# Kernel optimization log

Hardware: AMD Instinct MI355X
Metric: run time of the kernel (lower is better)

## Reference

```python
import jax, jax.numpy as jnp
import numpy as np

KS = 3   # kernel_size
PAD = 1  # padding
N_K = KS * KS


def conv2d(x, w, b=None, stride=1, pad=0):
    out = jax.lax.conv_general_dilated(
        x, w, (stride, stride), [(pad, pad), (pad, pad)],
        dimension_numbers=('NCHW', 'OIHW', 'NCHW'))
    if b is not None:
        out = out + b[None, :, None, None]
    return out


def deform_sample(x, offset):
    # x: [b,c,H,W]  offset: [b,2N,h,w] -> [b,c,h,w,N]
    b, c, H, W = x.shape
    _, twoN, h, w = offset.shape
    N = twoN // 2
    xp = jnp.pad(x, ((0, 0), (0, 0), (PAD, PAD), (PAD, PAD)))
    Hp, Wp = H + 2 * PAD, W + 2 * PAD
    r = (KS - 1) // 2
    knx, kny = jnp.meshgrid(jnp.arange(-r, r + 1), jnp.arange(-r, r + 1), indexing='ij')
    pnx = knx.reshape(-1).astype(offset.dtype)  # [N] kernel x offsets
    pny = kny.reshape(-1).astype(offset.dtype)
    off = jnp.transpose(offset, (0, 2, 3, 1))   # [b,h,w,2N]
    p0x = (jnp.arange(h) + PAD).astype(offset.dtype)
    p0y = (jnp.arange(w) + PAD).astype(offset.dtype)
    px = p0x[None, :, None, None] + pnx[None, None, None, :] + off[..., :N]  # [b,h,w,N]
    py = p0y[None, None, :, None] + pny[None, None, None, :] + off[..., N:]
    # q = p.detach().floor() in torch -> stop_gradient here
    flx = jnp.floor(jax.lax.stop_gradient(px))
    fly = jnp.floor(jax.lax.stop_gradient(py))
    qltx = jnp.clip(flx, 0, Hp - 1)
    qrbx = jnp.clip(flx + 1, 0, Hp - 1)
    qlty = jnp.clip(fly, 0, Wp - 1)
    qrby = jnp.clip(fly + 1, 0, Wp - 1)
    pxc = jnp.clip(px, 0, Hp - 1)
    pyc = jnp.clip(py, 0, Wp - 1)
    g_lt = (1 + (qltx - pxc)) * (1 + (qlty - pyc))
    g_rb = (1 - (qrbx - pxc)) * (1 - (qrby - pyc))
    g_lb = (1 - (qrbx - pxc)) * (1 + (qlty - pyc))
    g_rt = (1 + (qltx - pxc)) * (1 - (qrby - pyc))
    ix_lt, ix_rb = qltx.astype(jnp.int32), qrbx.astype(jnp.int32)
    iy_lt, iy_rb = qlty.astype(jnp.int32), qrby.astype(jnp.int32)

    def gather(ix, iy):
        def one(xb, ixb, iyb):
            return xb[:, ixb, iyb]  # [c,h,w,N]
        return jax.vmap(one)(xp, ix, iy)

    x_lt = gather(ix_lt, iy_lt)
    x_rb = gather(ix_rb, iy_rb)
    x_lb = gather(ix_rb, iy_lt)
    x_rt = gather(ix_lt, iy_rb)
    return (g_lt[:, None] * x_lt + g_rb[:, None] * x_rb
            + g_lb[:, None] * x_lb + g_rt[:, None] * x_rt)


def z_weight(z, mode):
    # cubic interpolation basis weights; z: [b,N,h,w] -> [b,1,h,w,N]
    if mode == '1':
        w = 1 - 11.0 / 6.0 * z + z ** 2 - 1.0 / 6.0 * z ** 3
    elif mode == '2':
        w = 3 * z - 2.5 * z ** 2 + 0.5 * z ** 3
    elif mode == '4':
        w = -1.5 * z + 2 * z ** 2 - 0.5 * z ** 3
    else:
        w = 1.0 / 3.0 * z - 0.5 * z ** 2 + 1.0 / 6.0 * z ** 3
    return jnp.transpose(w, (0, 2, 3, 1))[:, None]


def reshape_x_offset(xo):
    # [b,c,h,w,ks*ks] -> [b,c,h*ks,w*ks] (torch cat/view equivalent)
    b, c, h, w, _ = xo.shape
    xo = xo.reshape(b, c, h, w, KS, KS)          # N = g*ks + k
    xo = jnp.transpose(xo, (0, 1, 2, 4, 3, 5))   # (b,c,h,g,w,k)
    return xo.reshape(b, c, h * KS, w * KS)


def setup_inputs() -> dict:
    key = jax.random.key(0)
    ks = jax.random.split(key, 18)
    B, C, OSC, OUTC, H, W = 2, 64, 64, 64, 128, 128
    f = jax.random.normal
    inp = {
        'img1': f(ks[0], (B, C, H, W), jnp.float32),
        'img2': f(ks[1], (B, C, H, W), jnp.float32),
        'img4': f(ks[2], (B, C, H, W), jnp.float32),
        'img5': f(ks[3], (B, C, H, W), jnp.float32),
        'offset_source': f(ks[4], (B, OSC, H, W), jnp.float32),
        'w_pc1': f(ks[5], (2 * N_K, OSC, 5, 5), jnp.float32) * 0.01,
        'b_pc1': f(ks[6], (2 * N_K,), jnp.float32) * 0.01,
        'w_pc2': f(ks[7], (2 * N_K, OSC, 5, 5), jnp.float32) * 0.01,
        'b_pc2': f(ks[8], (2 * N_K,), jnp.float32) * 0.01,
        'w_pc4': f(ks[9], (2 * N_K, OSC, 5, 5), jnp.float32) * 0.01,
        'b_pc4': f(ks[10], (2 * N_K,), jnp.float32) * 0.01,
        'w_pc5': f(ks[11], (2 * N_K, OSC, 5, 5), jnp.float32) * 0.01,
        'b_pc5': f(ks[12], (2 * N_K,), jnp.float32) * 0.01,
        'w_z': f(ks[13], (N_K, OSC, 5, 5), jnp.float32) * 0.01,
        'b_z': f(ks[14], (N_K,), jnp.float32) * 0.01,
        'w_m': f(ks[15], (N_K, OSC, 5, 5), jnp.float32) * 0.01,
        'b_m': f(ks[16], (N_K,), jnp.float32) * 0.01,
        'w_conv': f(ks[17], (OUTC, C, KS, KS), jnp.float32) * 0.05,
    }
    return inp


def reference(img1, img2, img4, img5, offset_source,
              w_pc1, b_pc1, w_pc2, b_pc2, w_pc4, b_pc4, w_pc5, b_pc5,
              w_z, b_z, w_m, b_m, w_conv):
    off1 = conv2d(offset_source, w_pc1, b_pc1, pad=2)
    off2 = conv2d(offset_source, w_pc2, b_pc2, pad=2)
    off4 = conv2d(offset_source, w_pc4, b_pc4, pad=2)
    off5 = conv2d(offset_source, w_pc5, b_pc5, pad=2)
    z = 3.0 * jax.nn.sigmoid(conv2d(offset_source, w_z, b_z, pad=2))
    m = jax.nn.sigmoid(conv2d(offset_source, w_m, b_m, pad=2))
    f1 = deform_sample(img1, off1)
    f2 = deform_sample(img2, off2)
    f4 = deform_sample(img4, off4)
    f5 = deform_sample(img5, off5)
    central = (f1 * z_weight(z, '1') + f2 * z_weight(z, '2')
               + f4 * z_weight(z, '4') + f5 * z_weight(z, '5'))
    central = central * jnp.transpose(m, (0, 2, 3, 1))[:, None]
    out = conv2d(reshape_x_offset(central), w_conv, None, stride=KS)
    return out
```

## Files before the change

kernel.cpp:

```cpp
#include <hip/hip_runtime.h>
#include <hip/hip_bf16.h>
#include <math.h>

#define HWX 16384

typedef __attribute__((ext_vector_type(8))) short short8v;
typedef __attribute__((ext_vector_type(4))) float f32x4;

__device__ inline ushort f2bf(float x) {
    union { __hip_bfloat16 h; ushort u; } cv;
    cv.h = __float2bfloat16(x);
    return cv.u;
}

__global__ __launch_bounds__(256) void prep_kernel(
    const float* __restrict__ w1, const float* __restrict__ b1,
    const float* __restrict__ w2, const float* __restrict__ b2,
    const float* __restrict__ w4, const float* __restrict__ b4,
    const float* __restrict__ w5, const float* __restrict__ b5,
    const float* __restrict__ wz, const float* __restrict__ bz,
    const float* __restrict__ wm, const float* __restrict__ bm,
    const float* __restrict__ osrc, const float* __restrict__ wc,
    __hip_bfloat16* __restrict__ Wpk, float* __restrict__ bpack,
    __hip_bfloat16* __restrict__ osT, __hip_bfloat16* __restrict__ WcPk)
{
    const int bid = blockIdx.x;
    if (bid < 600) {
        const int idx = bid * 256 + threadIdx.x;
        if (idx < 96) {
            const int o = idx; float v = 0.f;
            if      (o < 18) v = b1[o];
            else if (o < 36) v = b2[o - 18];
            else if (o < 54) v = b4[o - 36];
            else if (o < 72) v = b5[o - 54];
            else if (o < 81) v = bz[o - 72];
            else if (o < 90) v = bm[o - 81];
            bpack[o] = v;
        }
        if (idx < 96 * 1600) {
            const int o   = idx / 1600;
            const int k   = idx - o * 1600;
            const int kyx = k >> 6;
            const int ic  = k & 63;
            const int off = ic * 25 + kyx;
            float v = 0.f;
            if      (o < 18) v = w1[o * 1600 + off];
            else if (o < 36) v = w2[(o - 18) * 1600 + off];
            else if (o < 54) v = w4[(o - 36) * 1600 + off];
            else if (o < 72) v = w5[(o - 54) * 1600 + off];
            else if (o < 81) v = wz[(o - 72) * 1600 + off];
            else if (o < 90) v = wm[(o - 81) * 1600 + off];
            Wpk[idx] = __float2bfloat16(v);
        }
    } else if (bid < 864) {
        const int blk = bid - 600;
        const int yy = blk % 132;
        const int b  = blk / 132;
        __hip_bfloat16* dst = osT + ((size_t)b * 132 + yy) * 132 * 64;
        for (int idx = threadIdx.x; idx < 132 * 64; idx += 256) {
            const int xx = idx >> 6;
            const int c  = idx & 63;
            float v = 0.f;
            if (yy >= 2 && yy < 130 && xx >= 2 && xx < 130)
                v = osrc[(((b << 6) + c) << 14) + ((yy - 2) << 7) + (xx - 2)];
            dst[idx] = __float2bfloat16(v);
        }
    } else {
        const int idx = (bid - 864) * 256 + threadIdx.x;
        if (idx < 36864) {
            const int oc  = idx / 576;
            const int cnp = idx - oc * 576;
            const int n   = cnp >> 6;
            const int c   = cnp & 63;
            WcPk[idx] = __float2bfloat16(wc[oc * 576 + c * 9 + n]);
        }
    }
}

__global__ __launch_bounds__(256) void conv_mfma_kernel(
    const __hip_bfloat16* __restrict__ Wpk,
    const float* __restrict__ bpack,
    const __hip_bfloat16* __restrict__ osT,
    float* __restrict__ offs, float* __restrict__ zbuf, float* __restrict__ mbuf)
{
    __shared__ __align__(16) ushort slab[5 * 68 * 64];
    __shared__ __align__(16) ushort wbuf[2][96 * 64];

    const int bx = blockIdx.x;
    const int y  = bx >> 1;
    const int x0 = (bx & 1) << 6;
    const int b  = blockIdx.y;
    const int t    = threadIdx.x;
    const int wv   = t >> 6;
    const int lane = t & 63;
    const int l15  = lane & 15;
    const int kgrp = lane >> 4;
    const int wm   = wv >> 1;
    const int wn   = wv & 1;

    const ushort* ob = (const ushort*)osT + (size_t)b * (132 * 132 * 64);
    const ushort* Wg = (const ushort*)Wpk;

    for (int c = t; c < 2720; c += 256) {
        const int r5  = c / 544;
        const int rem = c - r5 * 544;
        const int col = rem >> 3;
        const int cb  = rem & 7;
        const short8v v = *(const short8v*)(ob + (((y + r5) * 132 + x0 + col) << 6) + (cb << 3));
        const int slot = r5 * 544 + (col << 3) + (cb ^ (col & 7));
        *(short8v*)((char*)slab + slot * 16) = v;
    }

#define STAGE_W(kyx, bi)                                                       \
    _Pragma("unroll")                                                          \
    for (int it = 0; it < 3; ++it) {                                           \
        const int c  = it * 256 + t;                                           \
        const int oc = c >> 3, cb = c & 7;                                     \
        const ushort* src = Wg + oc * 1600 + (kyx) * 64 + ((cb ^ (oc & 7)) << 3); \
        __builtin_amdgcn_global_load_lds(                                      \
            (const __attribute__((address_space(1))) void*)src,                \
            (__attribute__((address_space(3))) void*)((char*)wbuf[bi] + (it * 256 + wv * 64) * 16), \
            16, 0, 0);                                                         \
    }

    STAGE_W(0, 0)
    __syncthreads();

    f32x4 acc[3][2];
    #pragma unroll
    for (int m = 0; m < 3; ++m)
        #pragma unroll
        for (int n = 0; n < 2; ++n) acc[m][n] = (f32x4){0.f, 0.f, 0.f, 0.f};

    for (int kyx = 0; kyx < 25; ++kyx) {
        const int bi = kyx & 1;
        if (kyx < 24) STAGE_W(kyx + 1, bi ^ 1)
        const int ky = kyx / 5, kx = kyx % 5;
        #pragma unroll
        for (int kc = 0; kc < 2; ++kc) {
            const int kcg = (kc << 2) + kgrp;
            short8v af[3], bf[2];
            #pragma unroll
            for (int m = 0; m < 3; ++m) {
                const int oc = wm * 48 + m * 16 + l15;
                af[m] = *(const short8v*)((char*)wbuf[bi] + ((oc << 3) + (kcg ^ (oc & 7))) * 16);
            }
            #pragma unroll
            for (int n = 0; n < 2; ++n) {
                const int col = wn * 32 + n * 16 + l15 + kx;
                bf[n] = *(const short8v*)((char*)slab + ((ky * 68 + col) * 8 + (kcg ^ (col & 7))) * 16);
            }
            #pragma unroll
            for (int m = 0; m < 3; ++m)
                #pragma unroll
                for (int n = 0; n < 2; ++n)
                    acc[m][n] = __builtin_amdgcn_mfma_f32_16x16x32_bf16(af[m], bf[n], acc[m][n], 0, 0, 0);
        }
        __syncthreads();
    }
#undef STAGE_W

    #pragma unroll
    for (int m = 0; m < 3; ++m) {
        const int ocb = wm * 48 + m * 16 + (kgrp << 2);
        #pragma unroll
        for (int n = 0; n < 2; ++n) {
            const int x = x0 + wn * 32 + n * 16 + l15;
            const int p = (y << 7) + x;
            #pragma unroll
            for (int r = 0; r < 4; ++r) {
                const int o = ocb + r;
                const float v = acc[m][n][r] + bpack[o];
                if (o < 72) {
                    const int i = o / 18, ch = o - i * 18;
                    offs[i * (2 * 18 * HWX) + (((b * 18) + ch) << 14) + p] = v;
                } else if (o < 81) {
                    zbuf[((b * 9 + (o - 72)) << 14) + p] = 3.f / (1.f + expf(-v));
                } else if (o < 90) {
                    mbuf[((b * 9 + (o - 81)) << 14) + p] = 1.f / (1.f + expf(-v));
                }
            }
        }
    }
}

__global__ __launch_bounds__(256) void transpose_kernel(
    const float* __restrict__ i0, const float* __restrict__ i1,
    const float* __restrict__ i2, const float* __restrict__ i3,
    ushort* __restrict__ imgT)
{
    const int img = blockIdx.z;
    const int b   = blockIdx.y;
    const int p0  = blockIdx.x << 6;
    const float* src = (img == 0) ? i0 : (img == 1) ? i1 : (img == 2) ? i2 : i3;

    __shared__ float tile[64][65];
    const int t = threadIdx.x;
    const int pp = t & 63, c0 = t >> 6;
    #pragma unroll
    for (int k = 0; k < 16; ++k) {
        const int c = (k << 2) + c0;
        tile[c][pp] = src[(((b << 6) + c) << 14) + p0 + pp];
    }
    __syncthreads();
    const int c2 = t & 31, pl = t >> 5;
    #pragma unroll
    for (int k = 0; k < 8; ++k) {
        const int pi = (k << 3) + pl;
        const uint packed = (uint)f2bf(tile[2 * c2][pi])
                          | ((uint)f2bf(tile[2 * c2 + 1][pi]) << 16);
        *(uint*)(imgT + ((size_t)(((img << 1) + b) << 14) + p0 + pi) * 64 + 2 * c2)
            = packed;
    }
}

__global__ __launch_bounds__(256, 5) void fused_kernel(
    const float* __restrict__ offs,
    const float* __restrict__ zbuf,
    const float* __restrict__ mbuf,
    const ushort* __restrict__ imgT,
    const __hip_bfloat16* __restrict__ WcPk,
    float* __restrict__ out)
{
    __shared__ __hip_bfloat16 s_sb[16 * 584];
    __shared__ uint4 s_tap[16 * 36];

    const int t   = threadIdx.x;
    const int pid = blockIdx.x;
    const int b   = pid >> 10;
    const int rem = pid & 1023;
    const int h   = rem >> 3;
    const int w0p = (rem & 7) << 4;

    for (int u = t; u < 576; u += 256) {
        const int px_  = u / 36;
        const int unit = u - px_ * 36;
        const int i    = unit / 9;
        const int n    = unit - i * 9;
        const int wcol = w0p + px_;
        const int p    = (h << 7) + wcol;

        const float* ob = offs + i * (2 * 18 * HWX) + ((b * 18) << 14);
        const float ox = ob[(n << 14) + p];
        const float oy = ob[((n + 9) << 14) + p];
        const float z  = zbuf[((b * 9 + n) << 14) + p];
        const float mm = mbuf[((b * 9 + n) << 14) + p];

        const float zc0 = (i == 0) ? 1.f : 0.f;
        const float zc1 = (i == 0) ? (-11.f / 6.f) : (i == 1) ? 3.f
                         : (i == 2) ? -1.5f : (1.f / 3.f);
        const float zc2 = (i == 0) ? 1.f : (i == 1) ? -2.5f
                         : (i == 2) ? 2.f : -0.5f;
        const float zc3 = (i == 0) ? (-1.f / 6.f) : (i == 1) ? 0.5f
                         : (i == 2) ? -0.5f : (1.f / 6.f);
        const float zw   = zc0 + z * (zc1 + z * (zc2 + z * zc3));
        const float coef = zw * mm;

        const float pxf = (float)(h + n / 3) + ox;
        const float pyf = (float)(wcol + n % 3) + oy;
        const float flx = floorf(pxf), fly = floorf(pyf);
        const float qltx = fminf(fmaxf(flx, 0.f), 129.f);
        const float qrbx = fminf(fmaxf(flx + 1.f, 0.f), 129.f);
        const float qlty = fminf(fmaxf(fly, 0.f), 129.f);
        const float qrby = fminf(fmaxf(fly + 1.f, 0.f), 129.f);
        const float pxc = fminf(fmaxf(pxf, 0.f), 129.f);
        const float pyc = fminf(fmaxf(pyf, 0.f), 129.f);
        const float gxl = 1.f + (qltx - pxc);
        const float gxr = 1.f - (qrbx - pxc);
        const float gyl = 1.f + (qlty - pyc);
        const float gyr = 1.f - (qrby - pyc);
        const int ixl = (int)qltx, ixr = (int)qrbx;
        const int iyl = (int)qlty, iyr = (int)qrby;

        uint i0_, i1_, i2_, i3_, u0_, u1_, u2_, u3_;
        auto mk = [&](int qx, int qy, float g, uint& ii, uint& ww) {
            const bool valid = (qx >= 1) && (qx <= 128) && (qy >= 1) && (qy <= 128);
            ii = valid ? (uint)(((qx - 1) << 7) + (qy - 1)) : 0u;
            ww = valid ? (uint)f2bf(g * coef) : 0u;
        };
        mk(ixl, iyl, gxl * gyl, i0_, u0_);
        mk(ixr, iyr, gxr * gyr, i1_, u1_);
        mk(ixr, iyl, gxr * gyl, i2_, u2_);
        mk(ixl, iyr, gxl * gyr, i3_, u3_);
        uint4 tp;
        tp.x = i0_ | (i1_ << 16);
        tp.y = i2_ | (i3_ << 16);
        tp.z = u0_ | (u1_ << 16);
        tp.w = u2_ | (u3_ << 16);
        s_tap[u] = tp;
    }
    __syncthreads();

    const int lane = t & 63;
    const int wv   = t >> 6;
    const int c8   = lane & 7;
    const int half = (lane >> 3) & 1;
    const int pxs  = lane >> 4;
    const int px   = (wv << 2) + pxs;
    const int tb   = px * 36;
    const int cByte = c8 << 4;

    #pragma unroll 2
    for (int n = 0; n < 9; ++n) {
        float s8[8];
        #pragma unroll
        for (int m = 0; m < 8; ++m) s8[m] = 0.f;

        #pragma unroll
        for (int i = 0; i < 4; ++i) {
            const uint4 tp = s_tap[tb + i * 9 + n];
            const uint  pair = half ? tp.y : tp.x;
            const uint  wpr  = half ? tp.w : tp.z;
            const float wA = __uint_as_float(wpr << 16);
            const float wB = __uint_as_float(wpr & 0xffff0000u);
            const char* ibl = (const char*)imgT + (((size_t)((i << 1) + b)) << 21) + cByte;
            {
                const uint4 v = *(const uint4*)(ibl + ((pair & 0xffffu) << 7));
                s8[0] = fmaf(wA, __uint_as_float(v.x << 16),         s8[0]);
                s8[1] = fmaf(wA, __uint_as_float(v.x & 0xffff0000u), s8[1]);
                s8[2] = fmaf(wA, __uint_as_float(v.y << 16),         s8[2]);
                s8[3] = fmaf(wA, __uint_as_float(v.y & 0xffff0000u), s8[3]);
                s8[4] = fmaf(wA, __uint_as_float(v.z << 16),         s8[4]);
                s8[5] = fmaf(wA, __uint_as_float(v.z & 0xffff0000u), s8[5]);
                s8[6] = fmaf(wA, __uint_as_float(v.w << 16),         s8[6]);
                s8[7] = fmaf(wA, __uint_as_float(v.w & 0xffff0000u), s8[7]);
            }
            {
                const uint4 v = *(const uint4*)(ibl + ((pair >> 16) << 7));
                s8[0] = fmaf(wB, __uint_as_float(v.x << 16),         s8[0]);
                s8[1] = fmaf(wB, __uint_as_float(v.x & 0xffff0000u), s8[1]);
                s8[2] = fmaf(wB, __uint_as_float(v.y << 16),         s8[2]);
                s8[3] = fmaf(wB, __uint_as_float(v.y & 0xffff0000u), s8[3]);
                s8[4] = fmaf(wB, __uint_as_float(v.z << 16),         s8[4]);
                s8[5] = fmaf(wB, __uint_as_float(v.z & 0xffff0000u), s8[5]);
                s8[6] = fmaf(wB, __uint_as_float(v.w << 16),         s8[6]);
                s8[7] = fmaf(wB, __uint_as_float(v.w & 0xffff0000u), s8[7]);
            }
        }

        #pragma unroll
        for (int m = 0; m < 8; ++m) s8[m] += __shfl_xor(s8[m], 8);

        if (half == 0) {
            uint4 pk;
            pk.x = (uint)f2bf(s8[0]) | ((uint)f2bf(s8[1]) << 16);
            pk.y = (uint)f2bf(s8[2]) | ((uint)f2bf(s8[3]) << 16);
            pk.z = (uint)f2bf(s8[4]) | ((uint)f2bf(s8[5]) << 16);
            pk.w = (uint)f2bf(s8[6]) | ((uint)f2bf(s8[7]) << 16);
            *(uint4*)((char*)s_sb + px * 1168 + n * 128 + cByte) = pk;
        }
    }
    __syncthreads();

    const int l15  = lane & 15;
    const int kgrp = lane >> 4;
    const ushort* Wb = (const ushort*)WcPk + (wv * 16 + l15) * 576 + kgrp * 8;
    const ushort* sb = (const ushort*)s_sb + l15 * 584 + kgrp * 8;

    f32x4 acc = {0.f, 0.f, 0.f, 0.f};
    #pragma unroll
    for (int ks = 0; ks < 18; ++ks) {
        const short8v a  = *(const short8v*)(Wb + ks * 32);
        const short8v bb = *(const short8v*)(sb + ks * 32);
        acc = __builtin_amdgcn_mfma_f32_16x16x32_bf16(a, bb, acc, 0, 0, 0);
    }

    const int p = (h << 7) + w0p + l15;
    #pragma unroll
    for (int r = 0; r < 4; ++r) {
        const int oc = wv * 16 + (kgrp << 2) + r;
        out[(((b << 6) + oc) << 14) + p] = acc[r];
    }
}

extern "C" void kernel_launch(void* const* d_in, const int* in_sizes, int n_in,
                              void* d_out, int out_size, void* d_ws, size_t ws_size,
                              hipStream_t stream) {
    (void)in_sizes; (void)n_in; (void)out_size; (void)ws_size;
    const float* img1  = (const float*)d_in[0];
    const float* img2  = (const float*)d_in[1];
    const float* img4  = (const float*)d_in[2];
    const float* img5  = (const float*)d_in[3];
    const float* osrc  = (const float*)d_in[4];
    const float* w_pc1 = (const float*)d_in[5];
    const float* b_pc1 = (const float*)d_in[6];
    const float* w_pc2 = (const float*)d_in[7];
    const float* b_pc2 = (const float*)d_in[8];
    const float* w_pc4 = (const float*)d_in[9];
    const float* b_pc4 = (const float*)d_in[10];
    const float* w_pc5 = (const float*)d_in[11];
    const float* b_pc5 = (const float*)d_in[12];
    const float* w_z   = (const float*)d_in[13];
    const float* b_z   = (const float*)d_in[14];
    const float* w_m   = (const float*)d_in[15];
    const float* b_m   = (const float*)d_in[16];
    const float* w_cv  = (const float*)d_in[17];
    float* out = (float*)d_out;

    float* wsf  = (float*)d_ws;
    float* offs = wsf;
    float* zbuf = wsf + 4 * 589824;
    float* mbuf = zbuf + 294912;
    float* WcTr = mbuf + 294912;
    float* imgTr = WcTr + 36864;

    __hip_bfloat16* WcPk  = (__hip_bfloat16*)WcTr;
    ushort*         imgTb = (ushort*)imgTr;

    __hip_bfloat16* Wpk   = (__hip_bfloat16*)imgTr;
    float*          bpack = imgTr + 76800;
    __hip_bfloat16* osT   = (__hip_bfloat16*)(imgTr + 76912);

    prep_kernel<<<dim3(1008), 256, 0, stream>>>(
        w_pc1, b_pc1, w_pc2, b_pc2, w_pc4, b_pc4, w_pc5, b_pc5,
        w_z, b_z, w_m, b_m, osrc, w_cv, Wpk, bpack, osT, WcPk);
    conv_mfma_kernel<<<dim3(256, 2), 256, 0, stream>>>(
        Wpk, bpack, osT, offs, zbuf, mbuf);
    transpose_kernel<<<dim3(256, 2, 4), 256, 0, stream>>>(img1, img2, img4, img5, imgTb);
    fused_kernel<<<dim3(2048), 256, 0, stream>>>(offs, zbuf, mbuf, imgTb, WcPk, out);
}
```

Baseline: 98.45 us.

## Software-pipeline deformable gather loads with inline asm and explicit vmcnt waits

Replaces the tap loop with a fully unrolled, double-buffered schedule. Each tap's eight bilinear-corner 16-byte loads are issued through inline asm global_load_dwordx4, one tap ahead of the FMA work on the previous tap, with s_waitcnt vmcnt and sched barriers to control ordering. The aim is to hide gather latency by keeping more loads in flight per wave. It also lowers the launch-bounds occupancy hint from 5 to 4 to leave registers for the extra buffered loads, trading occupancy for per-wave memory-level parallelism.

```diff
diff --git a/kernel.cpp b/kernel.cpp
--- a/kernel.cpp
+++ b/kernel.cpp
@@ -214,7 +214,9 @@
     }
 }
 
-__global__ __launch_bounds__(256, 5) void fused_kernel(
+#define UAF __uint_as_float
+
+__global__ __launch_bounds__(256, 4) void fused_kernel(
     const float* __restrict__ offs,
     const float* __restrict__ zbuf,
     const float* __restrict__ mbuf,
@@ -300,56 +302,106 @@
     const int tb   = px * 36;
     const int cByte = c8 << 4;
 
-    #pragma unroll 2
-    for (int n = 0; n < 9; ++n) {
-        float s8[8];
-        #pragma unroll
-        for (int m = 0; m < 8; ++m) s8[m] = 0.f;
-
-        #pragma unroll
-        for (int i = 0; i < 4; ++i) {
-            const uint4 tp = s_tap[tb + i * 9 + n];
-            const uint  pair = half ? tp.y : tp.x;
-            const uint  wpr  = half ? tp.w : tp.z;
-            const float wA = __uint_as_float(wpr << 16);
-            const float wB = __uint_as_float(wpr & 0xffff0000u);
-            const char* ibl = (const char*)imgT + (((size_t)((i << 1) + b)) << 21) + cByte;
-            {
-                const uint4 v = *(const uint4*)(ibl + ((pair & 0xffffu) << 7));
-                s8[0] = fmaf(wA, __uint_as_float(v.x << 16),         s8[0]);
-                s8[1] = fmaf(wA, __uint_as_float(v.x & 0xffff0000u), s8[1]);
-                s8[2] = fmaf(wA, __uint_as_float(v.y << 16),         s8[2]);
-                s8[3] = fmaf(wA, __uint_as_float(v.y & 0xffff0000u), s8[3]);
-                s8[4] = fmaf(wA, __uint_as_float(v.z << 16),         s8[4]);
-                s8[5] = fmaf(wA, __uint_as_float(v.z & 0xffff0000u), s8[5]);
-                s8[6] = fmaf(wA, __uint_as_float(v.w << 16),         s8[6]);
-                s8[7] = fmaf(wA, __uint_as_float(v.w & 0xffff0000u), s8[7]);
-            }
-            {
-                const uint4 v = *(const uint4*)(ibl + ((pair >> 16) << 7));
-                s8[0] = fmaf(wB, __uint_as_float(v.x << 16),         s8[0]);
-                s8[1] = fmaf(wB, __uint_as_float(v.x & 0xffff0000u), s8[1]);
-                s8[2] = fmaf(wB, __uint_as_float(v.y << 16),         s8[2]);
-                s8[3] = fmaf(wB, __uint_as_float(v.y & 0xffff0000u), s8[3]);
-                s8[4] = fmaf(wB, __uint_as_float(v.z << 16),         s8[4]);
-                s8[5] = fmaf(wB, __uint_as_float(v.z & 0xffff0000u), s8[5]);
-                s8[6] = fmaf(wB, __uint_as_float(v.w << 16),         s8[6]);
-                s8[7] = fmaf(wB, __uint_as_float(v.w & 0xffff0000u), s8[7]);
-            }
-        }
-
-        #pragma unroll
-        for (int m = 0; m < 8; ++m) s8[m] += __shfl_xor(s8[m], 8);
-
-        if (half == 0) {
-            uint4 pk;
-            pk.x = (uint)f2bf(s8[0]) | ((uint)f2bf(s8[1]) << 16);
-            pk.y = (uint)f2bf(s8[2]) | ((uint)f2bf(s8[3]) << 16);
-            pk.z = (uint)f2bf(s8[4]) | ((uint)f2bf(s8[5]) << 16);
-            pk.w = (uint)f2bf(s8[6]) | ((uint)f2bf(s8[7]) << 16);
-            *(uint4*)((char*)s_sb + px * 1168 + n * 128 + cByte) = pk;
-        }
-    }
+    const char* ibl0 = (const char*)imgT + (((size_t)(0 + b)) << 21) + cByte;
+    const char* ibl1 = (const char*)imgT + (((size_t)(2 + b)) << 21) + cByte;
+    const char* ibl2 = (const char*)imgT + (((size_t)(4 + b)) << 21) + cByte;
+    const char* ibl3 = (const char*)imgT + (((size_t)(6 + b)) << 21) + cByte;
+
+#define AI(n, V)                                                               \
+    uint4 V##r0, V##r1, V##r2, V##r3, V##r4, V##r5, V##r6, V##r7;              \
+    float V##w0, V##w1, V##w2, V##w3, V##w4, V##w5, V##w6, V##w7;              \
+    {                                                                          \
+        const uint4 t0 = s_tap[tb + 0 * 9 + (n)];                              \
+        const uint4 t1 = s_tap[tb + 1 * 9 + (n)];                              \
+        const uint4 t2 = s_tap[tb + 2 * 9 + (n)];                              \
+        const uint4 t3 = s_tap[tb + 3 * 9 + (n)];                              \
+        const uint p0 = half ? t0.y : t0.x, q0 = half ? t0.w : t0.z;           \
+        const uint p1 = half ? t1.y : t1.x, q1 = half ? t1.w : t1.z;           \
+        const uint p2 = half ? t2.y : t2.x, q2 = half ? t2.w : t2.z;           \
+        const uint p3 = half ? t3.y : t3.x, q3 = half ? t3.w : t3.z;           \
+        V##w0 = UAF(q0 << 16); V##w1 = UAF(q0 & 0xffff0000u);                  \
+        V##w2 = UAF(q1 << 16); V##w3 = UAF(q1 & 0xffff0000u);                  \
+        V##w4 = UAF(q2 << 16); V##w5 = UAF(q2 & 0xffff0000u);                  \
+        V##w6 = UAF(q3 << 16); V##w7 = UAF(q3 & 0xffff0000u);                  \
+        const char* a0 = ibl0 + ((p0 & 0xffffu) << 7);                         \
+        const char* a1 = ibl0 + ((p0 >> 16) << 7);                             \
+        const char* a2 = ibl1 + ((p1 & 0xffffu) << 7);                         \
+        const char* a3 = ibl1 + ((p1 >> 16) << 7);                             \
+        const char* a4 = ibl2 + ((p2 & 0xffffu) << 7);                         \
+        const char* a5 = ibl2 + ((p2 >> 16) << 7);                             \
+        const char* a6 = ibl3 + ((p3 & 0xffffu) << 7);                         \
+        const char* a7 = ibl3 + ((p3 >> 16) << 7);                             \
+        asm volatile(                                                          \
+            "global_load_dwordx4 %0, %8, off\n\t"                              \
+            "global_load_dwordx4 %1, %9, off\n\t"                              \
+            "global_load_dwordx4 %2, %10, off\n\t"                             \
+            "global_load_dwordx4 %3, %11, off\n\t"                             \
+            "global_load_dwordx4 %4, %12, off\n\t"                             \
+            "global_load_dwordx4 %5, %13, off\n\t"                             \
+            "global_load_dwordx4 %6, %14, off\n\t"                             \
+            "global_load_dwordx4 %7, %15, off"                                 \
+            : "=&v"(V##r0), "=&v"(V##r1), "=&v"(V##r2), "=&v"(V##r3),          \
+              "=&v"(V##r4), "=&v"(V##r5), "=&v"(V##r6), "=&v"(V##r7)           \
+            : "v"(a0), "v"(a1), "v"(a2), "v"(a3),                              \
+              "v"(a4), "v"(a5), "v"(a6), "v"(a7));                             \
+    }
+
+#define FMA8(Wf, Vr)                                                           \
+    s8[0] = fmaf(Wf, UAF((Vr).x << 16),         s8[0]);                        \
+    s8[1] = fmaf(Wf, UAF((Vr).x & 0xffff0000u), s8[1]);                        \
+    s8[2] = fmaf(Wf, UAF((Vr).y << 16),         s8[2]);                        \
+    s8[3] = fmaf(Wf, UAF((Vr).y & 0xffff0000u), s8[3]);                        \
+    s8[4] = fmaf(Wf, UAF((Vr).z << 16),         s8[4]);                        \
+    s8[5] = fmaf(Wf, UAF((Vr).z & 0xffff0000u), s8[5]);                        \
+    s8[6] = fmaf(Wf, UAF((Vr).w << 16),         s8[6]);                        \
+    s8[7] = fmaf(Wf, UAF((Vr).w & 0xffff0000u), s8[7]);
+
+#define PROC(n, V)                                                             \
+    {                                                                          \
+        float s8[8];                                                           \
+        _Pragma("unroll") for (int m = 0; m < 8; ++m) s8[m] = 0.f;             \
+        FMA8(V##w0, V##r0) FMA8(V##w1, V##r1) FMA8(V##w2, V##r2)               \
+        FMA8(V##w3, V##r3) FMA8(V##w4, V##r4) FMA8(V##w5, V##r5)               \
+        FMA8(V##w6, V##r6) FMA8(V##w7, V##r7)                                  \
+        _Pragma("unroll") for (int m = 0; m < 8; ++m)                          \
+            s8[m] += __shfl_xor(s8[m], 8);                                     \
+        if (half == 0) {                                                       \
+            uint4 pk;                                                          \
+            pk.x = (uint)f2bf(s8[0]) | ((uint)f2bf(s8[1]) << 16);              \
+            pk.y = (uint)f2bf(s8[2]) | ((uint)f2bf(s8[3]) << 16);              \
+            pk.z = (uint)f2bf(s8[4]) | ((uint)f2bf(s8[5]) << 16);              \
+            pk.w = (uint)f2bf(s8[6]) | ((uint)f2bf(s8[7]) << 16);              \
+            *(uint4*)((char*)s_sb + px * 1168 + (n) * 128 + cByte) = pk;       \
+        }                                                                      \
+    }
+
+#define WAITSB(N)                                                              \
+    asm volatile("s_waitcnt vmcnt(" #N ")" ::: "memory");                      \
+    __builtin_amdgcn_sched_barrier(0);
+
+    AI(0, g0)
+    AI(1, g1)
+    WAITSB(8)  PROC(0, g0)
+    AI(2, g2)
+    WAITSB(8)  PROC(1, g1)
+    AI(3, g3)
+    WAITSB(8)  PROC(2, g2)
+    AI(4, g4)
+    WAITSB(8)  PROC(3, g3)
+    AI(5, g5)
+    WAITSB(8)  PROC(4, g4)
+    AI(6, g6)
+    WAITSB(8)  PROC(5, g5)
+    AI(7, g7)
+    WAITSB(8)  PROC(6, g6)
+    AI(8, g8)
+    WAITSB(8)  PROC(7, g7)
+    WAITSB(0)  PROC(8, g8)
+
+#undef AI
+#undef FMA8
+#undef PROC
+#undef WAITSB
     __syncthreads();
 
     const int l15  = lane & 15;
```

Result: no change. 96.77 us (-1.7%).
